# Kernel tuning notes

Hardware: AMD Instinct MI355X
Metric: run time of the kernel (lower is better)

## Reference

```python
import jax, jax.numpy as jnp
import numpy as np

N, H, E, D, L = 100000, 20000, 1600000, 64, 3
F = 4 * D  # ffn hidden = out_dim * 4


def _ln(x, g, b, eps=1e-5):
    mu = x.mean(-1, keepdims=True)
    var = ((x - mu) ** 2).mean(-1, keepdims=True)
    return (x - mu) * jax.lax.rsqrt(var + eps) * g + b


def _gconv(x, W, b, src, dst, inv_sqrt_src, inv_sqrt_dst, n_dst):
    # DGL GraphConv, norm='both': D_dst^{-1/2} A D_src^{-1/2} (x W) + b
    h = (x * inv_sqrt_src[:, None]) @ W
    agg = jax.ops.segment_sum(h[src], dst, num_segments=n_dst)
    return agg * inv_sqrt_dst[:, None] + b


def setup_inputs() -> dict:
    key = jax.random.key(0)
    ks = jax.random.split(key, 24)
    s = 0.05
    inp = {
        'node_features': jax.random.normal(ks[0], (N, D), jnp.float32),
        'edge_src': jax.random.randint(ks[1], (E,), 0, N),
        'edge_dst': jax.random.randint(ks[2], (E,), 0, H),
        'n_hyper': H,
        # stacked per-layer params [L, ...]
        'Wn2h': jax.random.normal(ks[3], (L, D, D), jnp.float32) * s,
        'bn2h': jnp.zeros((L, D), jnp.float32),
        'Wh2n': jax.random.normal(ks[4], (L, D, D), jnp.float32) * s,
        'bh2n': jnp.zeros((L, D), jnp.float32),
        'W1': jax.random.normal(ks[5], (L, D, F), jnp.float32) * s,
        'b1': jnp.zeros((L, F), jnp.float32),
        'W2': jax.random.normal(ks[6], (L, F, D), jnp.float32) * s,
        'b2': jnp.zeros((L, D), jnp.float32),
        'g1': jnp.ones((L, D), jnp.float32),
        'be1': jnp.zeros((L, D), jnp.float32),
        'g2': jnp.ones((L, D), jnp.float32),
        'be2': jnp.zeros((L, D), jnp.float32),
        'gF': jnp.ones((D,), jnp.float32),
        'bF': jnp.zeros((D,), jnp.float32),
        'Wo': jax.random.normal(ks[7], (D, D), jnp.float32) * s,
        'bo': jnp.zeros((D,), jnp.float32),
    }
    return inp


def reference(node_features, edge_src, edge_dst, n_hyper, Wn2h, bn2h, Wh2n, bh2n,
              W1, b1, W2, b2, g1, be1, g2, be2, gF, bF, Wo, bo):
    n_nodes = node_features.shape[0]
    ones = jnp.ones(edge_src.shape[0], node_features.dtype)
    deg_node = jnp.clip(jax.ops.segment_sum(ones, edge_src, num_segments=n_nodes), 1.0)
    deg_hyp = jnp.clip(jax.ops.segment_sum(ones, edge_dst, num_segments=n_hyper), 1.0)
    is_node = jax.lax.rsqrt(deg_node)  # node out-degree^{-1/2}
    is_hyp = jax.lax.rsqrt(deg_hyp)    # hyperedge in-degree^{-1/2}

    def step(h, p):
        Wa, ba, Wb, bb, w1, c1, w2, c2, gg1, ee1, gg2, ee2 = p
        # node -> hyperedge conv (unused attention output is overwritten in the original)
        h_hyper = _gconv(h, Wa, ba, edge_src, edge_dst, is_node, is_hyp, n_hyper)
        # hyperedge -> node conv on reversed graph (degrees swap roles)
        h_node = _gconv(h_hyper, Wb, bb, edge_dst, edge_src, is_hyp, is_node, n_nodes)
        h = _ln(h + h_node, gg1, ee1)
        h_ffn = jax.nn.relu(h @ w1 + c1) @ w2 + c2
        h = _ln(h + h_ffn, gg2, ee2)
        return h, None

    h, _ = jax.lax.scan(step, node_features,
                        (Wn2h, bn2h, Wh2n, bh2n, W1, b1, W2, b2, g1, be1, g2, be2))
    h = _ln(h, gF, bF)
    return h @ Wo + bo
```

## Files before the change

### kernel.cpp

```cpp
#include <hip/hip_runtime.h>

#define HYP 20000
#define NLAYER 3
#define NB_H 313
#define NB_N 391
#define PT 4096

typedef __attribute__((ext_vector_type(8))) short short8;
typedef __attribute__((ext_vector_type(4))) float floatx4;

static __device__ __forceinline__ unsigned short f2bf(float f){
  union { float f; unsigned u; } v; v.f = f;
  unsigned r = v.u + 0x7FFF + ((v.u >> 16) & 1);
  return (unsigned short)(r >> 16);
}

__global__ __launch_bounds__(256) void k_hist(const int* __restrict__ src,
    const int* __restrict__ dst, int E, int* __restrict__ bh, int* __restrict__ bn){
  __shared__ int lh[NB_H + NB_N];
  int tid = threadIdx.x;
  for (int i = tid; i < NB_H + NB_N; i += 256) lh[i] = 0;
  __syncthreads();
  for (int i = blockIdx.x*256 + tid; i < E; i += gridDim.x*256){
    atomicAdd(&lh[dst[i] >> 6], 1);
    atomicAdd(&lh[NB_H + (src[i] >> 8)], 1);
  }
  __syncthreads();
  for (int i = tid; i < NB_H; i += 256) if (lh[i]) atomicAdd(&bh[i], lh[i]);
  for (int i = tid; i < NB_N; i += 256) if (lh[NB_H+i]) atomicAdd(&bn[i], lh[NB_H+i]);
}

__global__ __launch_bounds__(256) void k_bscan(const int* __restrict__ bh,
    const int* __restrict__ bn, int* __restrict__ bstart_h, int* __restrict__ gcur_h,
    int* __restrict__ bstart_n, int* __restrict__ gcur_n){
  __shared__ int ssc[4];
  __shared__ int scarry;
  int tid = threadIdx.x, lane = tid & 63, wv = tid >> 6;
  if (tid == 0) scarry = 0;
  __syncthreads();
  for (int base = 0; base < NB_H; base += 256){
    int i = base + tid; int v = (i < NB_H) ? bh[i] : 0; int x = v;
    #pragma unroll
    for (int o = 1; o < 64; o <<= 1){ int t = __shfl_up(x,o,64); if (lane >= o) x += t; }
    if (lane == 63) ssc[wv] = x;
    __syncthreads();
    int add = (wv>0?ssc[0]:0)+(wv>1?ssc[1]:0)+(wv>2?ssc[2]:0);
    int c = scarry;
    if (i < NB_H){ int ex = c + add + x - v; bstart_h[i] = ex; gcur_h[i] = ex; }
    __syncthreads();
    if (tid == 255) scarry = c + ssc[0]+ssc[1]+ssc[2]+ssc[3];
    __syncthreads();
  }
  if (tid == 0){ bstart_h[NB_H] = scarry; scarry = 0; }
  __syncthreads();
  for (int base = 0; base < NB_N; base += 256){
    int i = base + tid; int v = (i < NB_N) ? bn[i] : 0; int x = v;
    #pragma unroll
    for (int o = 1; o < 64; o <<= 1){ int t = __shfl_up(x,o,64); if (lane >= o) x += t; }
    if (lane == 63) ssc[wv] = x;
    __syncthreads();
    int add = (wv>0?ssc[0]:0)+(wv>1?ssc[1]:0)+(wv>2?ssc[2]:0);
    int c = scarry;
    if (i < NB_N){ int ex = c + add + x - v; bstart_n[i] = ex; gcur_n[i] = ex; }
    __syncthreads();
    if (tid == 255) scarry = c + ssc[0]+ssc[1]+ssc[2]+ssc[3];
    __syncthreads();
  }
  if (tid == 0) bstart_n[NB_N] = scarry;
}

__global__ __launch_bounds__(256) void k_partition(const int* __restrict__ keys,
    const int* __restrict__ pays, int E, int keyshift, int nb,
    int* __restrict__ gcur, unsigned* __restrict__ Ebuf){
  __shared__ unsigned sst[PT];
  __shared__ int lh[NB_N], lpre[NB_N], gb[NB_N];
  __shared__ int ssc[4];
  __shared__ int scarry;
  int tid = threadIdx.x, lane = tid & 63, wv = tid >> 6;
  int base = blockIdx.x*PT;
  int m = min(PT, E - base);
  for (int i = tid; i < nb; i += 256) lh[i] = 0;
  if (tid == 0) scarry = 0;
  __syncthreads();
  unsigned en[16]; int rk[16];
  #pragma unroll
  for (int j = 0; j < 16; ++j){
    int i = base + j*256 + tid;
    if (i < E){
      unsigned k = (unsigned)keys[i], p = (unsigned)pays[i];
      en[j] = (k << keyshift) | p;
      rk[j] = atomicAdd(&lh[en[j] >> 23], 1);
    } else { en[j] = 0; rk[j] = -1; }
  }
  __syncthreads();
  for (int b2 = 0; b2 < nb; b2 += 256){
    int i = b2 + tid; int v = (i < nb) ? lh[i] : 0; int x = v;
    #pragma unroll
    for (int o = 1; o < 64; o <<= 1){ int t = __shfl_up(x,o,64); if (lane >= o) x += t; }
    if (lane == 63) ssc[wv] = x;
    __syncthreads();
    int add = (wv>0?ssc[0]:0)+(wv>1?ssc[1]:0)+(wv>2?ssc[2]:0);
    int c = scarry;
    if (i < nb) lpre[i] = c + add + x - v;
    __syncthreads();
    if (tid == 255) scarry = c + ssc[0]+ssc[1]+ssc[2]+ssc[3];
    __syncthreads();
  }
  for (int i = tid; i < nb; i += 256) gb[i] = atomicAdd(&gcur[i], lh[i]);
  #pragma unroll
  for (int j = 0; j < 16; ++j){
    if (rk[j] >= 0){
      int bk = en[j] >> 23;
      sst[lpre[bk] + rk[j]] = en[j];
    }
  }
  __syncthreads();
  for (int j = tid; j < m; j += 256){
    unsigned e = sst[j];
    int bk = e >> 23;
    Ebuf[gb[bk] + (j - lpre[bk])] = e;
  }
}

__global__ __launch_bounds__(256) void k_build(const unsigned* __restrict__ Ebuf,
    const int* __restrict__ bstart, int keyshift, int ipb, int paymask, int limit,
    int* __restrict__ off, float* __restrict__ isv, int* __restrict__ csr){
  __shared__ int lcnt[256], lpre2[256], lcur[256];
  int tid = threadIdx.x, lane = tid & 63, wv = tid >> 6;
  int b = blockIdx.x;
  int base = bstart[b], m = bstart[b+1] - base;
  for (int i = tid; i < ipb; i += 256) lcnt[i] = 0;
  __syncthreads();
  for (int i = tid; i < m; i += 256){
    unsigned e = Ebuf[base + i];
    atomicAdd(&lcnt[(e >> keyshift) & (ipb-1)], 1);
  }
  __syncthreads();
  if (wv == 0){
    int carry = 0;
    for (int c = 0; c < ipb; c += 64){
      int li = c + lane;
      int v = lcnt[li]; int x = v;
      #pragma unroll
      for (int o = 1; o < 64; o <<= 1){ int t = __shfl_up(x,o,64); if (lane >= o) x += t; }
      int ex = carry + x - v;
      int id = b*ipb + li;
      if (id <= limit) off[id] = base + ex;
      if (id < limit) isv[id] = rsqrtf((float)(v > 0 ? v : 1));
      lpre2[li] = ex;
      carry += __shfl(x, 63, 64);
    }
  }
  for (int i = tid; i < ipb; i += 256) lcur[i] = 0;
  __syncthreads();
  for (int i = tid; i < m; i += 256){
    unsigned e = Ebuf[base + i];
    int li = (e >> keyshift) & (ipb-1);
    int pos = base + lpre2[li] + atomicAdd(&lcur[li], 1);
    csr[pos] = (int)(e & (unsigned)paymask);
  }
}

__global__ void k_prescale(const float* __restrict__ x, const float* __restrict__ isn,
                           unsigned short* __restrict__ xb, int nrows){
  int i = blockIdx.x*blockDim.x + threadIdx.x;
  int st = gridDim.x*blockDim.x;
  int tot = nrows*64;
  for (; i < tot; i += st){ xb[i] = f2bf(x[i]*isn[i >> 6]); }
}

__global__ void k_cvtall(const float* __restrict__ W1, const float* __restrict__ W2,
                         const float* __restrict__ Wa, const float* __restrict__ Wb,
                         const float* __restrict__ Wo,
                         unsigned short* __restrict__ W1T, unsigned short* __restrict__ W2T,
                         unsigned short* __restrict__ WaT, unsigned short* __restrict__ WbT,
                         unsigned short* __restrict__ WoT){
  int st = gridDim.x*blockDim.x;
  int t0 = blockIdx.x*blockDim.x + threadIdx.x;
  for (int j = t0; j < NLAYER*16384; j += st){
    int l = j >> 14, n = (j >> 6) & 255, k = j & 63;
    W1T[j] = f2bf(W1[l*16384 + k*256 + n]);
  }
  for (int j = t0; j < NLAYER*16384; j += st){
    int l = j >> 14, o = (j >> 8) & 63, kk = j & 255;
    W2T[j] = f2bf(W2[l*16384 + kk*64 + o]);
  }
  for (int j = t0; j < NLAYER*4096; j += st){
    int l = j >> 12, n = (j >> 6) & 63, k = j & 63;
    WaT[j] = f2bf(Wa[l*4096 + k*64 + n]);
  }
  for (int j = t0; j < NLAYER*4096; j += st){
    int l = j >> 12, n = (j >> 6) & 63, k = j & 63;
    WbT[j] = f2bf(Wb[l*4096 + k*64 + n]);
  }
  for (int j = t0; j < 4096; j += st){
    int n = (j >> 6) & 63, k = j & 63;
    WoT[j] = f2bf(Wo[k*64 + n]);
  }
}

template<int LSTR>
static __device__ __forceinline__ void stage64(const unsigned short* __restrict__ gsrc,
    unsigned short* __restrict__ ldst, int tid, int rows){
  int nch = rows*8;
  for (int idx = tid; idx < nch; idx += 256){
    int row = idx >> 3, kc = (idx & 7)*8;
    uint4 v = *(const uint4*)&gsrc[row*64 + kc];
    *(uint4*)&ldst[row*LSTR + kc] = v;
  }
}

__global__ __launch_bounds__(256) void k_gather8(const unsigned short* __restrict__ feat,
    const int* __restrict__ csr, const int* __restrict__ off,
    unsigned short* __restrict__ agg, int nrows){
  int lane = threadIdx.x & 63, wvi = threadIdx.x >> 6;
  int g = lane >> 3;
  int ch = (lane & 7) * 8;
  int r = blockIdx.x*4 + wvi, stride = gridDim.x*4;
  for (; r < nrows; r += stride){
    int b = off[r], e = off[r+1];
    float a0=0,a1=0,a2=0,a3=0,a4=0,a5=0,a6=0,a7=0;
    int t = b;
    for (; t + 16 <= e; t += 16){
      int s0 = csr[t + g];
      int s1 = csr[t + 8 + g];
      uint4 u0 = *(const uint4*)&feat[(size_t)s0*64 + ch];
      uint4 u1 = *(const uint4*)&feat[(size_t)s1*64 + ch];
      a0 += __uint_as_float(u0.x << 16); a1 += __uint_as_float(u0.x & 0xFFFF0000u);
      a2 += __uint_as_float(u0.y << 16); a3 += __uint_as_float(u0.y & 0xFFFF0000u);
      a4 += __uint_as_float(u0.z << 16); a5 += __uint_as_float(u0.z & 0xFFFF0000u);
      a6 += __uint_as_float(u0.w << 16); a7 += __uint_as_float(u0.w & 0xFFFF0000u);
      a0 += __uint_as_float(u1.x << 16); a1 += __uint_as_float(u1.x & 0xFFFF0000u);
      a2 += __uint_as_float(u1.y << 16); a3 += __uint_as_float(u1.y & 0xFFFF0000u);
      a4 += __uint_as_float(u1.z << 16); a5 += __uint_as_float(u1.z & 0xFFFF0000u);
      a6 += __uint_as_float(u1.w << 16); a7 += __uint_as_float(u1.w & 0xFFFF0000u);
    }
    for (; t < e; t += 8){
      int idx = t + g;
      bool valid = idx < e;
      int s = csr[valid ? idx : b];
      uint4 u = *(const uint4*)&feat[(size_t)s*64 + ch];
      if (!valid){ u.x = 0; u.y = 0; u.z = 0; u.w = 0; }
      a0 += __uint_as_float(u.x << 16); a1 += __uint_as_float(u.x & 0xFFFF0000u);
      a2 += __uint_as_float(u.y << 16); a3 += __uint_as_float(u.y & 0xFFFF0000u);
      a4 += __uint_as_float(u.z << 16); a5 += __uint_as_float(u.z & 0xFFFF0000u);
      a6 += __uint_as_float(u.w << 16); a7 += __uint_as_float(u.w & 0xFFFF0000u);
    }
    #pragma unroll
    for (int o = 8; o <= 32; o <<= 1){
      a0 += __shfl_xor(a0,o,64); a1 += __shfl_xor(a1,o,64);
      a2 += __shfl_xor(a2,o,64); a3 += __shfl_xor(a3,o,64);
      a4 += __shfl_xor(a4,o,64); a5 += __shfl_xor(a5,o,64);
      a6 += __shfl_xor(a6,o,64); a7 += __shfl_xor(a7,o,64);
    }
    if (g == 0){
      uint4 w;
      w.x = (unsigned)f2bf(a0) | ((unsigned)f2bf(a1) << 16);
      w.y = (unsigned)f2bf(a2) | ((unsigned)f2bf(a3) << 16);
      w.z = (unsigned)f2bf(a4) | ((unsigned)f2bf(a5) << 16);
      w.w = (unsigned)f2bf(a6) | ((unsigned)f2bf(a7) << 16);
      *(uint4*)&agg[(size_t)r*64 + ch] = w;
    }
  }
}

__global__ __launch_bounds__(256) void k_mmA(const unsigned short* __restrict__ aggb,
    const unsigned short* __restrict__ WaT, const float* __restrict__ bias,
    const float* __restrict__ ihy, unsigned short* __restrict__ ouths, int nrows){
  __shared__ unsigned short sWb[64*72];
  int tid = threadIdx.x;
  int lane = tid & 63, w = tid >> 6;
  int quad = lane >> 4, n16 = lane & 15;
  stage64<72>(WaT, sWb, tid, 64);
  __syncthreads();
  int rowbase = blockIdx.x*64 + w*16;
  int arow = min(rowbase + n16, nrows-1);
  short8 a0 = *(const short8*)&aggb[(size_t)arow*64 + quad*8];
  short8 a1 = *(const short8*)&aggb[(size_t)arow*64 + 32 + quad*8];
  float ih[4];
  #pragma unroll
  for (int r = 0; r < 4; ++r) ih[r] = ihy[min(rowbase + quad*4 + r, nrows-1)];
  #pragma unroll
  for (int ot = 0; ot < 4; ++ot){
    floatx4 c = (floatx4){0.f,0.f,0.f,0.f};
    short8 b0 = *(const short8*)&sWb[(ot*16+n16)*72 + quad*8];
    short8 b1 = *(const short8*)&sWb[(ot*16+n16)*72 + 32 + quad*8];
    c = __builtin_amdgcn_mfma_f32_16x16x32_bf16(a0, b0, c, 0, 0, 0);
    c = __builtin_amdgcn_mfma_f32_16x16x32_bf16(a1, b1, c, 0, 0, 0);
    float bl = bias[ot*16 + n16];
    #pragma unroll
    for (int r = 0; r < 4; ++r){
      int rr = rowbase + quad*4 + r;
      if (rr < nrows)
        ouths[(size_t)rr*64 + ot*16 + n16] = f2bf(fmaf(c[r], ih[r], bl) * ih[r]);
    }
  }
}

__global__ __launch_bounds__(256) void k_fused(
    const unsigned short* __restrict__ aggb,
    const unsigned short* __restrict__ WbT,
    const float* __restrict__ bbg,
    const float* __restrict__ isn,
    const float* __restrict__ hin,
    const float* __restrict__ g1v, const float* __restrict__ be1v,
    const unsigned short* __restrict__ W1T,
    const float* __restrict__ b1g,
    const unsigned short* __restrict__ W2T,
    const float* __restrict__ b2g,
    const float* __restrict__ g2v, const float* __restrict__ be2v,
    float* __restrict__ Outp, unsigned short* __restrict__ Qs, int nrows)
{
  __shared__ unsigned short sW1T[128*72];
  __shared__ unsigned short sW2T[64*136];
  __shared__ unsigned short sPH[4*16*72];
  unsigned short* sWb = sW1T;
  int tid = threadIdx.x;
  int lane = tid & 63, w = tid >> 6;
  int quad = lane >> 4, n16 = lane & 15;
  int rowbase = blockIdx.x*64 + w*16;

  stage64<72>(WbT, sWb, tid, 64);
  __syncthreads();

  int arow = min(rowbase + n16, nrows-1);
  short8 a0 = *(const short8*)&aggb[(size_t)arow*64 + quad*8];
  short8 a1 = *(const short8*)&aggb[(size_t)arow*64 + 32 + quad*8];
  floatx4 cB[4];
  #pragma unroll
  for (int ot = 0; ot < 4; ++ot){
    floatx4 c = (floatx4){0.f,0.f,0.f,0.f};
    short8 b0 = *(const short8*)&sWb[(ot*16+n16)*72 + quad*8];
    short8 b1 = *(const short8*)&sWb[(ot*16+n16)*72 + 32 + quad*8];
    c = __builtin_amdgcn_mfma_f32_16x16x32_bf16(a0, b0, c, 0, 0, 0);
    c = __builtin_amdgcn_mfma_f32_16x16x32_bf16(a1, b1, c, 0, 0, 0);
    cB[ot] = c;
  }

  float isr[4];
  #pragma unroll
  for (int r = 0; r < 4; ++r) isr[r] = isn[min(rowbase + quad*4 + r, nrows-1)];
  float pP[4][4];
  #pragma unroll
  for (int ot = 0; ot < 4; ++ot){
    float bb = bbg[ot*16 + n16];
    #pragma unroll
    for (int r = 0; r < 4; ++r){
      int rr = min(rowbase + quad*4 + r, nrows-1);
      pP[ot][r] = fmaf(cB[ot][r], isr[r], bb) + hin[(size_t)rr*64 + ot*16 + n16];
    }
  }
  {
    float gl[4], bl[4];
    #pragma unroll
    for (int ot = 0; ot < 4; ++ot){ gl[ot] = g1v[ot*16+n16]; bl[ot] = be1v[ot*16+n16]; }
    #pragma unroll
    for (int r = 0; r < 4; ++r){
      float s = (pP[0][r] + pP[1][r]) + (pP[2][r] + pP[3][r]);
      float q = fmaf(pP[0][r], pP[0][r], pP[1][r]*pP[1][r]) +
                fmaf(pP[2][r], pP[2][r], pP[3][r]*pP[3][r]);
      #pragma unroll
      for (int o = 8; o >= 1; o >>= 1){
        s += __shfl_xor(s, o, 64);
        q += __shfl_xor(q, o, 64);
      }
      float mu = s*(1.f/64.f);
      float var = fmaf(-mu, mu, q*(1.f/64.f));
      float rs = rsqrtf(var + 1e-5f);
      #pragma unroll
      for (int ot = 0; ot < 4; ++ot)
        pP[ot][r] = fmaf((pP[ot][r]-mu)*rs, gl[ot], bl[ot]);
    }
  }
  unsigned short* myP = &sPH[w*16*72];
  #pragma unroll
  for (int ot = 0; ot < 4; ++ot)
    #pragma unroll
    for (int r = 0; r < 4; ++r)
      myP[(quad*4 + r)*72 + ot*16 + n16] = f2bf(pP[ot][r]);
  short8 p0 = *(const short8*)&myP[n16*72 + quad*8];
  short8 p1 = *(const short8*)&myP[n16*72 + 32 + quad*8];

  floatx4 acc2[4];
  #pragma unroll
  for (int t = 0; t < 4; ++t) acc2[t] = (floatx4){0.f,0.f,0.f,0.f};
  unsigned short* myHc = &sPH[w*16*72];

  for (int hb = 0; hb < 2; ++hb){
    __syncthreads();
    stage64<72>(W1T + hb*128*64, sW1T, tid, 128);
    for (int idx = tid; idx < 1024; idx += 256){
      int o = idx >> 4, kc = (idx & 15)*8;
      uint4 v = *(const uint4*)&W2T[o*256 + hb*128 + kc];
      *(uint4*)&sW2T[o*136 + kc] = v;
    }
    __syncthreads();

    for (int ck = 0; ck < 4; ++ck){
      #pragma unroll
      for (int nt = 0; nt < 2; ++nt){
        int nn = ck*32 + nt*16 + n16;
        floatx4 c = (floatx4){0.f,0.f,0.f,0.f};
        short8 b0 = *(const short8*)&sW1T[nn*72 + quad*8];
        short8 b1f = *(const short8*)&sW1T[nn*72 + 32 + quad*8];
        c = __builtin_amdgcn_mfma_f32_16x16x32_bf16(p0, b0, c, 0, 0, 0);
        c = __builtin_amdgcn_mfma_f32_16x16x32_bf16(p1, b1f, c, 0, 0, 0);
        float bb = b1g[hb*128 + nn];
        #pragma unroll
        for (int r = 0; r < 4; ++r){
          float h = fmaxf(c[r] + bb, 0.f);
          myHc[(quad*4 + r)*40 + nt*16 + n16] = f2bf(h);
        }
      }
      short8 a2 = *(const short8*)&myHc[n16*40 + quad*8];
      #pragma unroll
      for (int ot = 0; ot < 4; ++ot){
        short8 b2f = *(const short8*)&sW2T[(ot*16 + n16)*136 + ck*32 + quad*8];
        acc2[ot] = __builtin_amdgcn_mfma_f32_16x16x32_bf16(a2, b2f, acc2[ot], 0, 0, 0);
      }
    }
  }

  float pre[4][4];
  #pragma unroll
  for (int ot = 0; ot < 4; ++ot){
    float b2c = b2g[ot*16 + n16];
    #pragma unroll
    for (int r = 0; r < 4; ++r)
      pre[ot][r] = acc2[ot][r] + b2c + pP[ot][r];
  }
  float gl[4], bel[4];
  #pragma unroll
  for (int ot = 0; ot < 4; ++ot){ gl[ot] = g2v[ot*16 + n16]; bel[ot] = be2v[ot*16 + n16]; }
  #pragma unroll
  for (int r = 0; r < 4; ++r){
    float s = (pre[0][r] + pre[1][r]) + (pre[2][r] + pre[3][r]);
    float q = fmaf(pre[0][r], pre[0][r], pre[1][r]*pre[1][r]) +
              fmaf(pre[2][r], pre[2][r], pre[3][r]*pre[3][r]);
    #pragma unroll
    for (int o = 8; o >= 1; o >>= 1){
      s += __shfl_xor(s, o, 64);
      q += __shfl_xor(q, o, 64);
    }
    float mu = s*(1.f/64.f);
    float var = fmaf(-mu, mu, q*(1.f/64.f));
    float rs = rsqrtf(var + 1e-5f);
    int rr = rowbase + quad*4 + r;
    if (rr < nrows){
      float isr2 = isn[rr];
      #pragma unroll
      for (int ot = 0; ot < 4; ++ot){
        float ov = fmaf((pre[ot][r]-mu)*rs, gl[ot], bel[ot]);
        Outp[(size_t)rr*64 + ot*16 + n16] = ov;
        Qs[(size_t)rr*64 + ot*16 + n16] = f2bf(ov * isr2);
      }
    }
  }
}

__global__ __launch_bounds__(256) void k_final(const float* __restrict__ Q,
    const unsigned short* __restrict__ WoT, const float* __restrict__ bog,
    const float* __restrict__ gF, const float* __restrict__ bF,
    float* __restrict__ out, int nrows){
  __shared__ unsigned short sWb[64*72];
  int tid = threadIdx.x;
  int lane = tid & 63, w = tid >> 6;
  int quad = lane >> 4, n16 = lane & 15;
  stage64<72>(WoT, sWb, tid, 64);
  __syncthreads();
  int rowbase = blockIdx.x*64 + w*16;
  int arow = min(rowbase + n16, nrows-1);
  float4 q0 = *(const float4*)&Q[(size_t)arow*64 + quad*8];
  float4 q1 = *(const float4*)&Q[(size_t)arow*64 + quad*8 + 4];
  float4 q2 = *(const float4*)&Q[(size_t)arow*64 + 32 + quad*8];
  float4 q3 = *(const float4*)&Q[(size_t)arow*64 + 32 + quad*8 + 4];
  float s = (q0.x+q0.y+q0.z+q0.w) + (q1.x+q1.y+q1.z+q1.w)
          + (q2.x+q2.y+q2.z+q2.w) + (q3.x+q3.y+q3.z+q3.w);
  float qq = (q0.x*q0.x+q0.y*q0.y+q0.z*q0.z+q0.w*q0.w)
           + (q1.x*q1.x+q1.y*q1.y+q1.z*q1.z+q1.w*q1.w)
           + (q2.x*q2.x+q2.y*q2.y+q2.z*q2.z+q2.w*q2.w)
           + (q3.x*q3.x+q3.y*q3.y+q3.z*q3.z+q3.w*q3.w);
  s += __shfl_xor(s, 16, 64);  qq += __shfl_xor(qq, 16, 64);
  s += __shfl_xor(s, 32, 64);  qq += __shfl_xor(qq, 32, 64);
  float mu = s*(1.f/64.f);
  float var = fmaf(-mu, mu, qq*(1.f/64.f));
  float rs = rsqrtf(var + 1e-5f);
  float4 g0 = *(const float4*)&gF[quad*8];
  float4 g1 = *(const float4*)&gF[quad*8 + 4];
  float4 g2 = *(const float4*)&gF[32 + quad*8];
  float4 g3 = *(const float4*)&gF[32 + quad*8 + 4];
  float4 f0 = *(const float4*)&bF[quad*8];
  float4 f1 = *(const float4*)&bF[quad*8 + 4];
  float4 f2 = *(const float4*)&bF[32 + quad*8];
  float4 f3 = *(const float4*)&bF[32 + quad*8 + 4];
  short8 a0, a1;
  a0[0]=f2bf(fmaf((q0.x-mu)*rs, g0.x, f0.x)); a0[1]=f2bf(fmaf((q0.y-mu)*rs, g0.y, f0.y));
  a0[2]=f2bf(fmaf((q0.z-mu)*rs, g0.z, f0.z)); a0[3]=f2bf(fmaf((q0.w-mu)*rs, g0.w, f0.w));
  a0[4]=f2bf(fmaf((q1.x-mu)*rs, g1.x, f1.x)); a0[5]=f2bf(fmaf((q1.y-mu)*rs, g1.y, f1.y));
  a0[6]=f2bf(fmaf((q1.z-mu)*rs, g1.z, f1.z)); a0[7]=f2bf(fmaf((q1.w-mu)*rs, g1.w, f1.w));
  a1[0]=f2bf(fmaf((q2.x-mu)*rs, g2.x, f2.x)); a1[1]=f2bf(fmaf((q2.y-mu)*rs, g2.y, f2.y));
  a1[2]=f2bf(fmaf((q2.z-mu)*rs, g2.z, f2.z)); a1[3]=f2bf(fmaf((q2.w-mu)*rs, g2.w, f2.w));
  a1[4]=f2bf(fmaf((q3.x-mu)*rs, g3.x, f3.x)); a1[5]=f2bf(fmaf((q3.y-mu)*rs, g3.y, f3.y));
  a1[6]=f2bf(fmaf((q3.z-mu)*rs, g3.z, f3.z)); a1[7]=f2bf(fmaf((q3.w-mu)*rs, g3.w, f3.w));
  #pragma unroll
  for (int ot = 0; ot < 4; ++ot){
    floatx4 c = (floatx4){0.f,0.f,0.f,0.f};
    short8 b0 = *(const short8*)&sWb[(ot*16+n16)*72 + quad*8];
    short8 b1 = *(const short8*)&sWb[(ot*16+n16)*72 + 32 + quad*8];
    c = __builtin_amdgcn_mfma_f32_16x16x32_bf16(a0, b0, c, 0, 0, 0);
    c = __builtin_amdgcn_mfma_f32_16x16x32_bf16(a1, b1, c, 0, 0, 0);
    float bol = bog[ot*16 + n16];
    #pragma unroll
    for (int r = 0; r < 4; ++r){
      int rr = rowbase + quad*4 + r;
      if (rr < nrows) out[(size_t)rr*64 + ot*16 + n16] = c[r] + bol;
    }
  }
}

extern "C" void kernel_launch(void* const* d_in, const int* in_sizes, int n_in,
                              void* d_out, int out_size, void* d_ws, size_t ws_size,
                              hipStream_t stream){
  const float* nf   = (const float*)d_in[0];
  const int*   esrc = (const int*)d_in[1];
  const int*   edst = (const int*)d_in[2];
  const float* Wn2h = (const float*)d_in[4];
  const float* bn2h = (const float*)d_in[5];
  const float* Wh2n = (const float*)d_in[6];
  const float* bh2n = (const float*)d_in[7];
  const float* W1   = (const float*)d_in[8];
  const float* b1   = (const float*)d_in[9];
  const float* W2   = (const float*)d_in[10];
  const float* b2   = (const float*)d_in[11];
  const float* g1   = (const float*)d_in[12];
  const float* be1  = (const float*)d_in[13];
  const float* g2   = (const float*)d_in[14];
  const float* be2  = (const float*)d_in[15];
  const float* gF   = (const float*)d_in[16];
  const float* bF   = (const float*)d_in[17];
  const float* Wo   = (const float*)d_in[18];
  const float* bo   = (const float*)d_in[19];
  const int N = in_sizes[0] / 64;
  const int E = in_sizes[1];
  const int H = HYP;
  float* out = (float*)d_out;

  char* w = (char*)d_ws;
  auto carve = [&](size_t bytes) -> char* {
    char* p = w; w += (bytes + 255) & ~(size_t)255; return p;
  };
  int* bh = (int*)carve((size_t)(NB_H + NB_N)*4);
  int* bn = bh + NB_H;
  int* bstart_h = (int*)carve((size_t)(NB_H+1)*4);
  int* gcur_h   = (int*)carve((size_t)NB_H*4);
  int* bstart_n = (int*)carve((size_t)(NB_N+1)*4);
  int* gcur_n   = (int*)carve((size_t)NB_N*4);
  unsigned* Ebuf_h = (unsigned*)carve((size_t)E*4);
  unsigned* Ebuf_n = (unsigned*)carve((size_t)E*4);
  int*   off_h = (int*)carve((size_t)(H+1)*4);
  int*   off_n = (int*)carve((size_t)(N+1)*4);
  float* is_h  = (float*)carve((size_t)H*4);
  float* is_n  = (float*)carve((size_t)N*4);
  int*   csr_h = (int*)carve((size_t)E*4);
  int*   csr_n = (int*)carve((size_t)E*4);
  unsigned short* aggxb = (unsigned short*)carve((size_t)H*64*2);
  unsigned short* agghb = (unsigned short*)carve((size_t)N*64*2);
  float* Qb    = (float*)carve((size_t)N*64*4);
  unsigned short* hhsb = (unsigned short*)carve((size_t)H*64*2);
  unsigned short* xb0  = (unsigned short*)carve((size_t)N*64*2);
  unsigned short* Qs   = (unsigned short*)carve((size_t)N*64*2);
  unsigned short* W1g16 = (unsigned short*)carve((size_t)NLAYER*64*256*2);
  unsigned short* W2g16 = (unsigned short*)carve((size_t)NLAYER*256*64*2);
  unsigned short* Wag16 = (unsigned short*)carve((size_t)NLAYER*4096*2);
  unsigned short* Wbg16 = (unsigned short*)carve((size_t)NLAYER*4096*2);
  unsigned short* Wog16 = (unsigned short*)carve((size_t)4096*2);

  hipMemsetAsync(bh, 0, (size_t)(NB_H + NB_N)*4, stream);
  k_cvtall<<<96, 256, 0, stream>>>(W1, W2, Wn2h, Wh2n, Wo,
                                   W1g16, W2g16, Wag16, Wbg16, Wog16);
  k_hist<<<512, 256, 0, stream>>>(esrc, edst, E, bh, bn);
  k_bscan<<<1, 256, 0, stream>>>(bh, bn, bstart_h, gcur_h, bstart_n, gcur_n);
  k_partition<<<(E + PT - 1)/PT, 256, 0, stream>>>(edst, esrc, E, 17, NB_H, gcur_h, Ebuf_h);
  k_partition<<<(E + PT - 1)/PT, 256, 0, stream>>>(esrc, edst, E, 15, NB_N, gcur_n, Ebuf_n);
  k_build<<<NB_H, 256, 0, stream>>>(Ebuf_h, bstart_h, 17, 64, 0x1FFFF, H, off_h, is_h, csr_h);
  k_build<<<NB_N, 256, 0, stream>>>(Ebuf_n, bstart_n, 15, 256, 0x7FFF, N, off_n, is_n, csr_n);
  k_prescale<<<4096, 256, 0, stream>>>(nf, is_n, xb0, N);

  const int NB64 = (N + 63)/64;
  const int HB64 = (H + 63)/64;
  for (int l = 0; l < NLAYER; ++l){
    const float* hin = (l == 0) ? nf : Qb;
    const unsigned short* hsrc = (l == 0) ? xb0 : Qs;
    k_gather8<<<2048, 256, 0, stream>>>(hsrc, csr_h, off_h, aggxb, H);
    k_mmA<<<HB64, 256, 0, stream>>>(aggxb, Wag16 + l*4096, bn2h + l*64, is_h, hhsb, H);
    k_gather8<<<2048, 256, 0, stream>>>(hhsb, csr_n, off_n, agghb, N);
    k_fused<<<NB64, 256, 0, stream>>>(agghb, Wbg16 + l*4096, bh2n + l*64, is_n, hin,
                                      g1 + l*64, be1 + l*64,
                                      W1g16 + l*64*256, b1 + l*256,
                                      W2g16 + l*256*64, b2 + l*64,
                                      g2 + l*64, be2 + l*64, Qb, Qs, N);
  }
  k_final<<<NB64, 256, 0, stream>>>(Qb, Wog16, bo, gF, bF, out, N);
}
```

Measured before the change: 538.0 us.

## Process two row tiles per wave in fused FFN kernel; unroll gather by 32

The fused post-aggregation kernel now handles 128 rows per block, two 16-row subtiles per wave. The staged Wb, W1 and W2 weights in LDS are reused across both subtiles, which halves the weight staging and block count. The hyperedge gather loop also gains a 32-edge unrolled stage so more feature loads are in flight at once. The cost is higher register pressure, which may reduce occupancy, and fewer blocks across the GPU.

```diff
diff --git a/kernel.cpp b/kernel.cpp
--- a/kernel.cpp
+++ b/kernel.cpp
@@ -210,6 +210,12 @@
   }
 }
 
+#define ACC8(u) \
+  a0 += __uint_as_float(u.x << 16); a1 += __uint_as_float(u.x & 0xFFFF0000u); \
+  a2 += __uint_as_float(u.y << 16); a3 += __uint_as_float(u.y & 0xFFFF0000u); \
+  a4 += __uint_as_float(u.z << 16); a5 += __uint_as_float(u.z & 0xFFFF0000u); \
+  a6 += __uint_as_float(u.w << 16); a7 += __uint_as_float(u.w & 0xFFFF0000u);
+
 __global__ __launch_bounds__(256) void k_gather8(const unsigned short* __restrict__ feat,
     const int* __restrict__ csr, const int* __restrict__ off,
     unsigned short* __restrict__ agg, int nrows){
@@ -221,19 +227,23 @@
     int b = off[r], e = off[r+1];
     float a0=0,a1=0,a2=0,a3=0,a4=0,a5=0,a6=0,a7=0;
     int t = b;
+    for (; t + 32 <= e; t += 32){
+      int s0 = csr[t + g];
+      int s1 = csr[t + 8 + g];
+      int s2 = csr[t + 16 + g];
+      int s3 = csr[t + 24 + g];
+      uint4 u0 = *(const uint4*)&feat[(size_t)s0*64 + ch];
+      uint4 u1 = *(const uint4*)&feat[(size_t)s1*64 + ch];
+      uint4 u2 = *(const uint4*)&feat[(size_t)s2*64 + ch];
+      uint4 u3 = *(const uint4*)&feat[(size_t)s3*64 + ch];
+      ACC8(u0); ACC8(u1); ACC8(u2); ACC8(u3);
+    }
     for (; t + 16 <= e; t += 16){
       int s0 = csr[t + g];
       int s1 = csr[t + 8 + g];
       uint4 u0 = *(const uint4*)&feat[(size_t)s0*64 + ch];
       uint4 u1 = *(const uint4*)&feat[(size_t)s1*64 + ch];
-      a0 += __uint_as_float(u0.x << 16); a1 += __uint_as_float(u0.x & 0xFFFF0000u);
-      a2 += __uint_as_float(u0.y << 16); a3 += __uint_as_float(u0.y & 0xFFFF0000u);
-      a4 += __uint_as_float(u0.z << 16); a5 += __uint_as_float(u0.z & 0xFFFF0000u);
-      a6 += __uint_as_float(u0.w << 16); a7 += __uint_as_float(u0.w & 0xFFFF0000u);
-      a0 += __uint_as_float(u1.x << 16); a1 += __uint_as_float(u1.x & 0xFFFF0000u);
-      a2 += __uint_as_float(u1.y << 16); a3 += __uint_as_float(u1.y & 0xFFFF0000u);
-      a4 += __uint_as_float(u1.z << 16); a5 += __uint_as_float(u1.z & 0xFFFF0000u);
-      a6 += __uint_as_float(u1.w << 16); a7 += __uint_as_float(u1.w & 0xFFFF0000u);
+      ACC8(u0); ACC8(u1);
     }
     for (; t < e; t += 8){
       int idx = t + g;
@@ -241,10 +251,7 @@
       int s = csr[valid ? idx : b];
       uint4 u = *(const uint4*)&feat[(size_t)s*64 + ch];
       if (!valid){ u.x = 0; u.y = 0; u.z = 0; u.w = 0; }
-      a0 += __uint_as_float(u.x << 16); a1 += __uint_as_float(u.x & 0xFFFF0000u);
-      a2 += __uint_as_float(u.y << 16); a3 += __uint_as_float(u.y & 0xFFFF0000u);
-      a4 += __uint_as_float(u.z << 16); a5 += __uint_as_float(u.z & 0xFFFF0000u);
-      a6 += __uint_as_float(u.w << 16); a7 += __uint_as_float(u.w & 0xFFFF0000u);
+      ACC8(u);
     }
     #pragma unroll
     for (int o = 8; o <= 32; o <<= 1){
@@ -304,10 +311,8 @@
     const float* __restrict__ isn,
     const float* __restrict__ hin,
     const float* __restrict__ g1v, const float* __restrict__ be1v,
-    const unsigned short* __restrict__ W1T,
-    const float* __restrict__ b1g,
-    const unsigned short* __restrict__ W2T,
-    const float* __restrict__ b2g,
+    const unsigned short* __restrict__ W1T, const float* __restrict__ b1g,
+    const unsigned short* __restrict__ W2T, const float* __restrict__ b2g,
     const float* __restrict__ g2v, const float* __restrict__ be2v,
     float* __restrict__ Outp, unsigned short* __restrict__ Qs, int nrows)
 {
@@ -318,36 +323,35 @@
   int tid = threadIdx.x;
   int lane = tid & 63, w = tid >> 6;
   int quad = lane >> 4, n16 = lane & 15;
-  int rowbase = blockIdx.x*64 + w*16;
+  int rb[2];
+  rb[0] = blockIdx.x*128 + w*16;
+  rb[1] = rb[0] + 64;
 
   stage64<72>(WbT, sWb, tid, 64);
   __syncthreads();
 
-  int arow = min(rowbase + n16, nrows-1);
-  short8 a0 = *(const short8*)&aggb[(size_t)arow*64 + quad*8];
-  short8 a1 = *(const short8*)&aggb[(size_t)arow*64 + 32 + quad*8];
-  floatx4 cB[4];
-  #pragma unroll
-  for (int ot = 0; ot < 4; ++ot){
-    floatx4 c = (floatx4){0.f,0.f,0.f,0.f};
-    short8 b0 = *(const short8*)&sWb[(ot*16+n16)*72 + quad*8];
-    short8 b1 = *(const short8*)&sWb[(ot*16+n16)*72 + 32 + quad*8];
-    c = __builtin_amdgcn_mfma_f32_16x16x32_bf16(a0, b0, c, 0, 0, 0);
-    c = __builtin_amdgcn_mfma_f32_16x16x32_bf16(a1, b1, c, 0, 0, 0);
-    cB[ot] = c;
-  }
-
-  float isr[4];
-  #pragma unroll
-  for (int r = 0; r < 4; ++r) isr[r] = isn[min(rowbase + quad*4 + r, nrows-1)];
-  float pP[4][4];
-  #pragma unroll
-  for (int ot = 0; ot < 4; ++ot){
-    float bb = bbg[ot*16 + n16];
-    #pragma unroll
-    for (int r = 0; r < 4; ++r){
-      int rr = min(rowbase + quad*4 + r, nrows-1);
-      pP[ot][r] = fmaf(cB[ot][r], isr[r], bb) + hin[(size_t)rr*64 + ot*16 + n16];
+  float pP[2][4][4];
+  float isr[2][4];
+  #pragma unroll
+  for (int s = 0; s < 2; ++s){
+    int arow = min(rb[s] + n16, nrows-1);
+    short8 a0 = *(const short8*)&aggb[(size_t)arow*64 + quad*8];
+    short8 a1 = *(const short8*)&aggb[(size_t)arow*64 + 32 + quad*8];
+    #pragma unroll
+    for (int r = 0; r < 4; ++r) isr[s][r] = isn[min(rb[s] + quad*4 + r, nrows-1)];
+    #pragma unroll
+    for (int ot = 0; ot < 4; ++ot){
+      floatx4 c = (floatx4){0.f,0.f,0.f,0.f};
+      short8 b0 = *(const short8*)&sWb[(ot*16+n16)*72 + quad*8];
+      short8 b1 = *(const short8*)&sWb[(ot*16+n16)*72 + 32 + quad*8];
+      c = __builtin_amdgcn_mfma_f32_16x16x32_bf16(a0, b0, c, 0, 0, 0);
+      c = __builtin_amdgcn_mfma_f32_16x16x32_bf16(a1, b1, c, 0, 0, 0);
+      float bb = bbg[ot*16 + n16];
+      #pragma unroll
+      for (int r = 0; r < 4; ++r){
+        int rr = min(rb[s] + quad*4 + r, nrows-1);
+        pP[s][ot][r] = fmaf(c[r], isr[s][r], bb) + hin[(size_t)rr*64 + ot*16 + n16];
+      }
     }
   }
   {
@@ -355,35 +359,43 @@
     #pragma unroll
     for (int ot = 0; ot < 4; ++ot){ gl[ot] = g1v[ot*16+n16]; bl[ot] = be1v[ot*16+n16]; }
     #pragma unroll
-    for (int r = 0; r < 4; ++r){
-      float s = (pP[0][r] + pP[1][r]) + (pP[2][r] + pP[3][r]);
-      float q = fmaf(pP[0][r], pP[0][r], pP[1][r]*pP[1][r]) +
-                fmaf(pP[2][r], pP[2][r], pP[3][r]*pP[3][r]);
+    for (int s = 0; s < 2; ++s)
       #pragma unroll
-      for (int o = 8; o >= 1; o >>= 1){
-        s += __shfl_xor(s, o, 64);
-        q += __shfl_xor(q, o, 64);
+      for (int r = 0; r < 4; ++r){
+        float sv = (pP[s][0][r] + pP[s][1][r]) + (pP[s][2][r] + pP[s][3][r]);
+        float q = fmaf(pP[s][0][r], pP[s][0][r], pP[s][1][r]*pP[s][1][r]) +
+                  fmaf(pP[s][2][r], pP[s][2][r], pP[s][3][r]*pP[s][3][r]);
+        #pragma unroll
+        for (int o = 8; o >= 1; o >>= 1){
+          sv += __shfl_xor(sv, o, 64);
+          q  += __shfl_xor(q, o, 64);
+        }
+        float mu = sv*(1.f/64.f);
+        float var = fmaf(-mu, mu, q*(1.f/64.f));
+        float rs = rsqrtf(var + 1e-5f);
+        #pragma unroll
+        for (int ot = 0; ot < 4; ++ot)
+          pP[s][ot][r] = fmaf((pP[s][ot][r]-mu)*rs, gl[ot], bl[ot]);
       }
-      float mu = s*(1.f/64.f);
-      float var = fmaf(-mu, mu, q*(1.f/64.f));
-      float rs = rsqrtf(var + 1e-5f);
+  }
+  unsigned short* myP = &sPH[w*16*72];
+  short8 p0[2], p1[2];
+  #pragma unroll
+  for (int s = 0; s < 2; ++s){
+    #pragma unroll
+    for (int ot = 0; ot < 4; ++ot)
       #pragma unroll
-      for (int ot = 0; ot < 4; ++ot)
-        pP[ot][r] = fmaf((pP[ot][r]-mu)*rs, gl[ot], bl[ot]);
-    }
-  }
-  unsigned short* myP = &sPH[w*16*72];
-  #pragma unroll
-  for (int ot = 0; ot < 4; ++ot)
-    #pragma unroll
-    for (int r = 0; r < 4; ++r)
-      myP[(quad*4 + r)*72 + ot*16 + n16] = f2bf(pP[ot][r]);
-  short8 p0 = *(const short8*)&myP[n16*72 + quad*8];
-  short8 p1 = *(const short8*)&myP[n16*72 + 32 + quad*8];
-
-  floatx4 acc2[4];
-  #pragma unroll
-  for (int t = 0; t < 4; ++t) acc2[t] = (floatx4){0.f,0.f,0.f,0.f};
+      for (int r = 0; r < 4; ++r)
+        myP[(quad*4 + r)*72 + ot*16 + n16] = f2bf(pP[s][ot][r]);
+    p0[s] = *(const short8*)&myP[n16*72 + quad*8];
+    p1[s] = *(const short8*)&myP[n16*72 + 32 + quad*8];
+  }
+
+  floatx4 acc2[2][4];
+  #pragma unroll
+  for (int s = 0; s < 2; ++s)
+    #pragma unroll
+    for (int t = 0; t < 4; ++t) acc2[s][t] = (floatx4){0.f,0.f,0.f,0.f};
   unsigned short* myHc = &sPH[w*16*72];
 
   for (int hb = 0; hb < 2; ++hb){
@@ -398,61 +410,67 @@
 
     for (int ck = 0; ck < 4; ++ck){
       #pragma unroll
-      for (int nt = 0; nt < 2; ++nt){
-        int nn = ck*32 + nt*16 + n16;
-        floatx4 c = (floatx4){0.f,0.f,0.f,0.f};
-        short8 b0 = *(const short8*)&sW1T[nn*72 + quad*8];
-        short8 b1f = *(const short8*)&sW1T[nn*72 + 32 + quad*8];
-        c = __builtin_amdgcn_mfma_f32_16x16x32_bf16(p0, b0, c, 0, 0, 0);
-        c = __builtin_amdgcn_mfma_f32_16x16x32_bf16(p1, b1f, c, 0, 0, 0);
-        float bb = b1g[hb*128 + nn];
+      for (int s = 0; s < 2; ++s){
         #pragma unroll
-        for (int r = 0; r < 4; ++r){
-          float h = fmaxf(c[r] + bb, 0.f);
-          myHc[(quad*4 + r)*40 + nt*16 + n16] = f2bf(h);
+        for (int nt = 0; nt < 2; ++nt){
+          int nn = ck*32 + nt*16 + n16;
+          floatx4 c = (floatx4){0.f,0.f,0.f,0.f};
+          short8 b0 = *(const short8*)&sW1T[nn*72 + quad*8];
+          short8 b1f = *(const short8*)&sW1T[nn*72 + 32 + quad*8];
+          c = __builtin_amdgcn_mfma_f32_16x16x32_bf16(p0[s], b0, c, 0, 0, 0);
+          c = __builtin_amdgcn_mfma_f32_16x16x32_bf16(p1[s], b1f, c, 0, 0, 0);
+          float bb = b1g[hb*128 + nn];
+          #pragma unroll
+          for (int r = 0; r < 4; ++r){
+            float h = fmaxf(c[r] + bb, 0.f);
+            myHc[(quad*4 + r)*40 + nt*16 + n16] = f2bf(h);
+          }
+        }
+        short8 a2 = *(const short8*)&myHc[n16*40 + quad*8];
+        #pragma unroll
+        for (int ot = 0; ot < 4; ++ot){
+          short8 b2f = *(const short8*)&sW2T[(ot*16 + n16)*136 + ck*32 + quad*8];
+          acc2[s][ot] = __builtin_amdgcn_mfma_f32_16x16x32_bf16(a2, b2f, acc2[s][ot], 0, 0, 0);
         }
       }
-      short8 a2 = *(const short8*)&myHc[n16*40 + quad*8];
+    }
+  }
+
+  float gl[4], bel[4];
+  #pragma unroll
+  for (int ot = 0; ot < 4; ++ot){ gl[ot] = g2v[ot*16 + n16]; bel[ot] = be2v[ot*16 + n16]; }
+  #pragma unroll
+  for (int s = 0; s < 2; ++s){
+    float pre[4][4];
+    #pragma unroll
+    for (int ot = 0; ot < 4; ++ot){
+      float b2c = b2g[ot*16 + n16];
       #pragma unroll
-      for (int ot = 0; ot < 4; ++ot){
-        short8 b2f = *(const short8*)&sW2T[(ot*16 + n16)*136 + ck*32 + quad*8];
-        acc2[ot] = __builtin_amdgcn_mfma_f32_16x16x32_bf16(a2, b2f, acc2[ot], 0, 0, 0);
+      for (int r = 0; r < 4; ++r)
+        pre[ot][r] = acc2[s][ot][r] + b2c + pP[s][ot][r];
+    }
+    #pragma unroll
+    for (int r = 0; r < 4; ++r){
+      float sv = (pre[0][r] + pre[1][r]) + (pre[2][r] + pre[3][r]);
+      float q = fmaf(pre[0][r], pre[0][r], pre[1][r]*pre[1][r]) +
+                fmaf(pre[2][r], pre[2][r], pre[3][r]*pre[3][r]);
+      #pragma unroll
+      for (int o = 8; o >= 1; o >>= 1){
+        sv += __shfl_xor(sv, o, 64);
+        q  += __shfl_xor(q, o, 64);
       }
-    }
-  }
-
-  float pre[4][4];
-  #pragma unroll
-  for (int ot = 0; ot < 4; ++ot){
-    float b2c = b2g[ot*16 + n16];
-    #pragma unroll
-    for (int r = 0; r < 4; ++r)
-      pre[ot][r] = acc2[ot][r] + b2c + pP[ot][r];
-  }
-  float gl[4], bel[4];
-  #pragma unroll
-  for (int ot = 0; ot < 4; ++ot){ gl[ot] = g2v[ot*16 + n16]; bel[ot] = be2v[ot*16 + n16]; }
-  #pragma unroll
-  for (int r = 0; r < 4; ++r){
-    float s = (pre[0][r] + pre[1][r]) + (pre[2][r] + pre[3][r]);
-    float q = fmaf(pre[0][r], pre[0][r], pre[1][r]*pre[1][r]) +
-              fmaf(pre[2][r], pre[2][r], pre[3][r]*pre[3][r]);
-    #pragma unroll
-    for (int o = 8; o >= 1; o >>= 1){
-      s += __shfl_xor(s, o, 64);
-      q += __shfl_xor(q, o, 64);
-    }
-    float mu = s*(1.f/64.f);
-    float var = fmaf(-mu, mu, q*(1.f/64.f));
-    float rs = rsqrtf(var + 1e-5f);
-    int rr = rowbase + quad*4 + r;
-    if (rr < nrows){
-      float isr2 = isn[rr];
-      #pragma unroll
-      for (int ot = 0; ot < 4; ++ot){
-        float ov = fmaf((pre[ot][r]-mu)*rs, gl[ot], bel[ot]);
-        Outp[(size_t)rr*64 + ot*16 + n16] = ov;
-        Qs[(size_t)rr*64 + ot*16 + n16] = f2bf(ov * isr2);
+      float mu = sv*(1.f/64.f);
+      float var = fmaf(-mu, mu, q*(1.f/64.f));
+      float rs = rsqrtf(var + 1e-5f);
+      int rr = rb[s] + quad*4 + r;
+      if (rr < nrows){
+        float isr2 = isn[rr];
+        #pragma unroll
+        for (int ot = 0; ot < 4; ++ot){
+          float ov = fmaf((pre[ot][r]-mu)*rs, gl[ot], bel[ot]);
+          Outp[(size_t)rr*64 + ot*16 + n16] = ov;
+          Qs[(size_t)rr*64 + ot*16 + n16] = f2bf(ov * isr2);
+        }
       }
     }
   }
@@ -587,6 +605,7 @@
   k_prescale<<<4096, 256, 0, stream>>>(nf, is_n, xb0, N);
 
   const int NB64 = (N + 63)/64;
+  const int NB128 = (N + 127)/128;
   const int HB64 = (H + 63)/64;
   for (int l = 0; l < NLAYER; ++l){
     const float* hin = (l == 0) ? nf : Qb;
@@ -594,11 +613,11 @@
     k_gather8<<<2048, 256, 0, stream>>>(hsrc, csr_h, off_h, aggxb, H);
     k_mmA<<<HB64, 256, 0, stream>>>(aggxb, Wag16 + l*4096, bn2h + l*64, is_h, hhsb, H);
     k_gather8<<<2048, 256, 0, stream>>>(hhsb, csr_n, off_n, agghb, N);
-    k_fused<<<NB64, 256, 0, stream>>>(agghb, Wbg16 + l*4096, bh2n + l*64, is_n, hin,
-                                      g1 + l*64, be1 + l*64,
-                                      W1g16 + l*64*256, b1 + l*256,
-                                      W2g16 + l*256*64, b2 + l*64,
-                                      g2 + l*64, be2 + l*64, Qb, Qs, N);
+    k_fused<<<NB128, 256, 0, stream>>>(agghb, Wbg16 + l*4096, bh2n + l*64, is_n, hin,
+                                       g1 + l*64, be1 + l*64,
+                                       W1g16 + l*64*256, b1 + l*256,
+                                       W2g16 + l*256*64, b2 + l*64,
+                                       g2 + l*64, be2 + l*64, Qb, Qs, N);
   }
   k_final<<<NB64, 256, 0, stream>>>(Qb, Wog16, bo, gF, bF, out, N);
 }
```

Measured after the change: 535.1 us. No clear change (-0.6%).

## Read MFMA weight fragments directly from global memory and unroll gather by 32

Applied to the files above, without the earlier changes.

Removes LDS staging of the weight matrices in k_mmA, k_fused and k_final. MFMA B fragments now load straight from global memory (L1/L2-cached), which drops __syncthreads barriers and frees LDS for higher occupancy. k_fused also loses its two-phase W1/W2 staging loop and walks all 256 hidden units in one loop. Separately, the gather kernel gains a 32-edge unrolled loop for more memory-level parallelism, with the repeated accumulation factored into a macro. The risk is that every wave now issues its own global weight loads, which adds cache traffic and latency inside the MFMA loop.

```diff
diff --git a/kernel.cpp b/kernel.cpp
--- a/kernel.cpp
+++ b/kernel.cpp
@@ -199,16 +199,11 @@
   }
 }
 
-template<int LSTR>
-static __device__ __forceinline__ void stage64(const unsigned short* __restrict__ gsrc,
-    unsigned short* __restrict__ ldst, int tid, int rows){
-  int nch = rows*8;
-  for (int idx = tid; idx < nch; idx += 256){
-    int row = idx >> 3, kc = (idx & 7)*8;
-    uint4 v = *(const uint4*)&gsrc[row*64 + kc];
-    *(uint4*)&ldst[row*LSTR + kc] = v;
-  }
-}
+#define ACC8(u) \
+  a0 += __uint_as_float(u.x << 16); a1 += __uint_as_float(u.x & 0xFFFF0000u); \
+  a2 += __uint_as_float(u.y << 16); a3 += __uint_as_float(u.y & 0xFFFF0000u); \
+  a4 += __uint_as_float(u.z << 16); a5 += __uint_as_float(u.z & 0xFFFF0000u); \
+  a6 += __uint_as_float(u.w << 16); a7 += __uint_as_float(u.w & 0xFFFF0000u);
 
 __global__ __launch_bounds__(256) void k_gather8(const unsigned short* __restrict__ feat,
     const int* __restrict__ csr, const int* __restrict__ off,
@@ -221,19 +216,23 @@
     int b = off[r], e = off[r+1];
     float a0=0,a1=0,a2=0,a3=0,a4=0,a5=0,a6=0,a7=0;
     int t = b;
+    for (; t + 32 <= e; t += 32){
+      int s0 = csr[t + g];
+      int s1 = csr[t + 8 + g];
+      int s2 = csr[t + 16 + g];
+      int s3 = csr[t + 24 + g];
+      uint4 u0 = *(const uint4*)&feat[(size_t)s0*64 + ch];
+      uint4 u1 = *(const uint4*)&feat[(size_t)s1*64 + ch];
+      uint4 u2 = *(const uint4*)&feat[(size_t)s2*64 + ch];
+      uint4 u3 = *(const uint4*)&feat[(size_t)s3*64 + ch];
+      ACC8(u0); ACC8(u1); ACC8(u2); ACC8(u3);
+    }
     for (; t + 16 <= e; t += 16){
       int s0 = csr[t + g];
       int s1 = csr[t + 8 + g];
       uint4 u0 = *(const uint4*)&feat[(size_t)s0*64 + ch];
       uint4 u1 = *(const uint4*)&feat[(size_t)s1*64 + ch];
-      a0 += __uint_as_float(u0.x << 16); a1 += __uint_as_float(u0.x & 0xFFFF0000u);
-      a2 += __uint_as_float(u0.y << 16); a3 += __uint_as_float(u0.y & 0xFFFF0000u);
-      a4 += __uint_as_float(u0.z << 16); a5 += __uint_as_float(u0.z & 0xFFFF0000u);
-      a6 += __uint_as_float(u0.w << 16); a7 += __uint_as_float(u0.w & 0xFFFF0000u);
-      a0 += __uint_as_float(u1.x << 16); a1 += __uint_as_float(u1.x & 0xFFFF0000u);
-      a2 += __uint_as_float(u1.y << 16); a3 += __uint_as_float(u1.y & 0xFFFF0000u);
-      a4 += __uint_as_float(u1.z << 16); a5 += __uint_as_float(u1.z & 0xFFFF0000u);
-      a6 += __uint_as_float(u1.w << 16); a7 += __uint_as_float(u1.w & 0xFFFF0000u);
+      ACC8(u0); ACC8(u1);
     }
     for (; t < e; t += 8){
       int idx = t + g;
@@ -241,10 +240,7 @@
       int s = csr[valid ? idx : b];
       uint4 u = *(const uint4*)&feat[(size_t)s*64 + ch];
       if (!valid){ u.x = 0; u.y = 0; u.z = 0; u.w = 0; }
-      a0 += __uint_as_float(u.x << 16); a1 += __uint_as_float(u.x & 0xFFFF0000u);
-      a2 += __uint_as_float(u.y << 16); a3 += __uint_as_float(u.y & 0xFFFF0000u);
-      a4 += __uint_as_float(u.z << 16); a5 += __uint_as_float(u.z & 0xFFFF0000u);
-      a6 += __uint_as_float(u.w << 16); a7 += __uint_as_float(u.w & 0xFFFF0000u);
+      ACC8(u);
     }
     #pragma unroll
     for (int o = 8; o <= 32; o <<= 1){
@@ -267,12 +263,9 @@
 __global__ __launch_bounds__(256) void k_mmA(const unsigned short* __restrict__ aggb,
     const unsigned short* __restrict__ WaT, const float* __restrict__ bias,
     const float* __restrict__ ihy, unsigned short* __restrict__ ouths, int nrows){
-  __shared__ unsigned short sWb[64*72];
   int tid = threadIdx.x;
   int lane = tid & 63, w = tid >> 6;
   int quad = lane >> 4, n16 = lane & 15;
-  stage64<72>(WaT, sWb, tid, 64);
-  __syncthreads();
   int rowbase = blockIdx.x*64 + w*16;
   int arow = min(rowbase + n16, nrows-1);
   short8 a0 = *(const short8*)&aggb[(size_t)arow*64 + quad*8];
@@ -283,8 +276,8 @@
   #pragma unroll
   for (int ot = 0; ot < 4; ++ot){
     floatx4 c = (floatx4){0.f,0.f,0.f,0.f};
-    short8 b0 = *(const short8*)&sWb[(ot*16+n16)*72 + quad*8];
-    short8 b1 = *(const short8*)&sWb[(ot*16+n16)*72 + 32 + quad*8];
+    short8 b0 = *(const short8*)&WaT[(ot*16+n16)*64 + quad*8];
+    short8 b1 = *(const short8*)&WaT[(ot*16+n16)*64 + 32 + quad*8];
     c = __builtin_amdgcn_mfma_f32_16x16x32_bf16(a0, b0, c, 0, 0, 0);
     c = __builtin_amdgcn_mfma_f32_16x16x32_bf16(a1, b1, c, 0, 0, 0);
     float bl = bias[ot*16 + n16];
@@ -311,43 +304,31 @@
     const float* __restrict__ g2v, const float* __restrict__ be2v,
     float* __restrict__ Outp, unsigned short* __restrict__ Qs, int nrows)
 {
-  __shared__ unsigned short sW1T[128*72];
-  __shared__ unsigned short sW2T[64*136];
   __shared__ unsigned short sPH[4*16*72];
-  unsigned short* sWb = sW1T;
   int tid = threadIdx.x;
   int lane = tid & 63, w = tid >> 6;
   int quad = lane >> 4, n16 = lane & 15;
   int rowbase = blockIdx.x*64 + w*16;
 
-  stage64<72>(WbT, sWb, tid, 64);
-  __syncthreads();
-
   int arow = min(rowbase + n16, nrows-1);
   short8 a0 = *(const short8*)&aggb[(size_t)arow*64 + quad*8];
   short8 a1 = *(const short8*)&aggb[(size_t)arow*64 + 32 + quad*8];
-  floatx4 cB[4];
+  float pP[4][4];
+  float isr[4];
+  #pragma unroll
+  for (int r = 0; r < 4; ++r) isr[r] = isn[min(rowbase + quad*4 + r, nrows-1)];
   #pragma unroll
   for (int ot = 0; ot < 4; ++ot){
     floatx4 c = (floatx4){0.f,0.f,0.f,0.f};
-    short8 b0 = *(const short8*)&sWb[(ot*16+n16)*72 + quad*8];
-    short8 b1 = *(const short8*)&sWb[(ot*16+n16)*72 + 32 + quad*8];
+    short8 b0 = *(const short8*)&WbT[(ot*16+n16)*64 + quad*8];
+    short8 b1 = *(const short8*)&WbT[(ot*16+n16)*64 + 32 + quad*8];
     c = __builtin_amdgcn_mfma_f32_16x16x32_bf16(a0, b0, c, 0, 0, 0);
     c = __builtin_amdgcn_mfma_f32_16x16x32_bf16(a1, b1, c, 0, 0, 0);
-    cB[ot] = c;
-  }
-
-  float isr[4];
-  #pragma unroll
-  for (int r = 0; r < 4; ++r) isr[r] = isn[min(rowbase + quad*4 + r, nrows-1)];
-  float pP[4][4];
-  #pragma unroll
-  for (int ot = 0; ot < 4; ++ot){
     float bb = bbg[ot*16 + n16];
     #pragma unroll
     for (int r = 0; r < 4; ++r){
       int rr = min(rowbase + quad*4 + r, nrows-1);
-      pP[ot][r] = fmaf(cB[ot][r], isr[r], bb) + hin[(size_t)rr*64 + ot*16 + n16];
+      pP[ot][r] = fmaf(c[r], isr[r], bb) + hin[(size_t)rr*64 + ot*16 + n16];
     }
   }
   {
@@ -356,15 +337,15 @@
     for (int ot = 0; ot < 4; ++ot){ gl[ot] = g1v[ot*16+n16]; bl[ot] = be1v[ot*16+n16]; }
     #pragma unroll
     for (int r = 0; r < 4; ++r){
-      float s = (pP[0][r] + pP[1][r]) + (pP[2][r] + pP[3][r]);
+      float sv = (pP[0][r] + pP[1][r]) + (pP[2][r] + pP[3][r]);
       float q = fmaf(pP[0][r], pP[0][r], pP[1][r]*pP[1][r]) +
                 fmaf(pP[2][r], pP[2][r], pP[3][r]*pP[3][r]);
       #pragma unroll
       for (int o = 8; o >= 1; o >>= 1){
-        s += __shfl_xor(s, o, 64);
-        q += __shfl_xor(q, o, 64);
+        sv += __shfl_xor(sv, o, 64);
+        q  += __shfl_xor(q, o, 64);
       }
-      float mu = s*(1.f/64.f);
+      float mu = sv*(1.f/64.f);
       float var = fmaf(-mu, mu, q*(1.f/64.f));
       float rs = rsqrtf(var + 1e-5f);
       #pragma unroll
@@ -386,38 +367,27 @@
   for (int t = 0; t < 4; ++t) acc2[t] = (floatx4){0.f,0.f,0.f,0.f};
   unsigned short* myHc = &sPH[w*16*72];
 
-  for (int hb = 0; hb < 2; ++hb){
-    __syncthreads();
-    stage64<72>(W1T + hb*128*64, sW1T, tid, 128);
-    for (int idx = tid; idx < 1024; idx += 256){
-      int o = idx >> 4, kc = (idx & 15)*8;
-      uint4 v = *(const uint4*)&W2T[o*256 + hb*128 + kc];
-      *(uint4*)&sW2T[o*136 + kc] = v;
-    }
-    __syncthreads();
-
-    for (int ck = 0; ck < 4; ++ck){
+  for (int ck = 0; ck < 8; ++ck){
+    #pragma unroll
+    for (int nt = 0; nt < 2; ++nt){
+      int nn = ck*32 + nt*16 + n16;
+      floatx4 c = (floatx4){0.f,0.f,0.f,0.f};
+      short8 b0 = *(const short8*)&W1T[nn*64 + quad*8];
+      short8 b1f = *(const short8*)&W1T[nn*64 + 32 + quad*8];
+      c = __builtin_amdgcn_mfma_f32_16x16x32_bf16(p0, b0, c, 0, 0, 0);
+      c = __builtin_amdgcn_mfma_f32_16x16x32_bf16(p1, b1f, c, 0, 0, 0);
+      float bb = b1g[nn];
       #pragma unroll
-      for (int nt = 0; nt < 2; ++nt){
-        int nn = ck*32 + nt*16 + n16;
-        floatx4 c = (floatx4){0.f,0.f,0.f,0.f};
-        short8 b0 = *(const short8*)&sW1T[nn*72 + quad*8];
-        short8 b1f = *(const short8*)&sW1T[nn*72 + 32 + quad*8];
-        c = __builtin_amdgcn_mfma_f32_16x16x32_bf16(p0, b0, c, 0, 0, 0);
-        c = __builtin_amdgcn_mfma_f32_16x16x32_bf16(p1, b1f, c, 0, 0, 0);
-        float bb = b1g[hb*128 + nn];
-        #pragma unroll
-        for (int r = 0; r < 4; ++r){
-          float h = fmaxf(c[r] + bb, 0.f);
-          myHc[(quad*4 + r)*40 + nt*16 + n16] = f2bf(h);
-        }
+      for (int r = 0; r < 4; ++r){
+        float h = fmaxf(c[r] + bb, 0.f);
+        myHc[(quad*4 + r)*40 + nt*16 + n16] = f2bf(h);
       }
-      short8 a2 = *(const short8*)&myHc[n16*40 + quad*8];
-      #pragma unroll
-      for (int ot = 0; ot < 4; ++ot){
-        short8 b2f = *(const short8*)&sW2T[(ot*16 + n16)*136 + ck*32 + quad*8];
-        acc2[ot] = __builtin_amdgcn_mfma_f32_16x16x32_bf16(a2, b2f, acc2[ot], 0, 0, 0);
-      }
+    }
+    short8 a2 = *(const short8*)&myHc[n16*40 + quad*8];
+    #pragma unroll
+    for (int ot = 0; ot < 4; ++ot){
+      short8 b2f = *(const short8*)&W2T[(ot*16 + n16)*256 + ck*32 + quad*8];
+      acc2[ot] = __builtin_amdgcn_mfma_f32_16x16x32_bf16(a2, b2f, acc2[ot], 0, 0, 0);
     }
   }
 
@@ -434,15 +404,15 @@
   for (int ot = 0; ot < 4; ++ot){ gl[ot] = g2v[ot*16 + n16]; bel[ot] = be2v[ot*16 + n16]; }
   #pragma unroll
   for (int r = 0; r < 4; ++r){
-    float s = (pre[0][r] + pre[1][r]) + (pre[2][r] + pre[3][r]);
+    float sv = (pre[0][r] + pre[1][r]) + (pre[2][r] + pre[3][r]);
     float q = fmaf(pre[0][r], pre[0][r], pre[1][r]*pre[1][r]) +
               fmaf(pre[2][r], pre[2][r], pre[3][r]*pre[3][r]);
     #pragma unroll
     for (int o = 8; o >= 1; o >>= 1){
-      s += __shfl_xor(s, o, 64);
-      q += __shfl_xor(q, o, 64);
-    }
-    float mu = s*(1.f/64.f);
+      sv += __shfl_xor(sv, o, 64);
+      q  += __shfl_xor(q, o, 64);
+    }
+    float mu = sv*(1.f/64.f);
     float var = fmaf(-mu, mu, q*(1.f/64.f));
     float rs = rsqrtf(var + 1e-5f);
     int rr = rowbase + quad*4 + r;
@@ -462,12 +432,9 @@
     const unsigned short* __restrict__ WoT, const float* __restrict__ bog,
     const float* __restrict__ gF, const float* __restrict__ bF,
     float* __restrict__ out, int nrows){
-  __shared__ unsigned short sWb[64*72];
   int tid = threadIdx.x;
   int lane = tid & 63, w = tid >> 6;
   int quad = lane >> 4, n16 = lane & 15;
-  stage64<72>(WoT, sWb, tid, 64);
-  __syncthreads();
   int rowbase = blockIdx.x*64 + w*16;
   int arow = min(rowbase + n16, nrows-1);
   float4 q0 = *(const float4*)&Q[(size_t)arow*64 + quad*8];
@@ -505,8 +472,8 @@
   #pragma unroll
   for (int ot = 0; ot < 4; ++ot){
     floatx4 c = (floatx4){0.f,0.f,0.f,0.f};
-    short8 b0 = *(const short8*)&sWb[(ot*16+n16)*72 + quad*8];
-    short8 b1 = *(const short8*)&sWb[(ot*16+n16)*72 + 32 + quad*8];
+    short8 b0 = *(const short8*)&WoT[(ot*16+n16)*64 + quad*8];
+    short8 b1 = *(const short8*)&WoT[(ot*16+n16)*64 + 32 + quad*8];
     c = __builtin_amdgcn_mfma_f32_16x16x32_bf16(a0, b0, c, 0, 0, 0);
     c = __builtin_amdgcn_mfma_f32_16x16x32_bf16(a1, b1, c, 0, 0, 0);
     float bol = bog[ot*16 + n16];
```

Result: slower. 625.5 us (+16.3%).
